# Kernel tuning notes

Measured on AMD Instinct MI355X. Metric: run time of the kernel, lower is better.

The kernel has to match this reference:

```python
import jax, jax.numpy as jnp
import numpy as np


def setup_inputs() -> dict:
    key = jax.random.key(0)
    k1, k2 = jax.random.split(key)
    x = jax.random.normal(k1, (32, 128, 112, 112), dtype=jnp.float32)
    weight = jax.random.normal(k2, (256, 128, 3, 3), dtype=jnp.float32)
    return {"x": x, "weight": weight}


def reference(x, weight):
    # Equivalent to torch unfold + einsum: valid (no padding), stride-1
    # cross-correlation conv2d with no bias.
    # x: [B, Cin, H, W], weight: [Cout, Cin, kh, kw] -> [B, Cout, H-kh+1, W-kw+1]
    return jax.lax.conv_general_dilated(
        x, weight,
        window_strides=(1, 1),
        padding="VALID",
        dimension_numbers=("NCHW", "OIHW", "NCHW"),
    )
```

## Files before the change

kernel.cpp:

```cpp
#include <hip/hip_runtime.h>

typedef __attribute__((ext_vector_type(8))) short short8;
typedef __attribute__((ext_vector_type(4))) float f32x4;
typedef unsigned int u32;

#define CIN   128
#define COUT  256
#define H     112
#define W     112
#define OH    110
#define OW    110
#define KHW   9
#define TH    8
#define TW    32
#define IWW   34
#define NPIX  340
#define XB    (NPIX*8*16)
#define WB    16384
#define ROWB  (IWW*128)

__device__ __forceinline__ short f2b(float f) {
  unsigned u = __builtin_bit_cast(unsigned, f);
  unsigned r = (u + 0x7FFFu + ((u >> 16) & 1u)) >> 16;
  return (short)r;
}

__device__ __forceinline__ void gload16(const void* g, void* l) {
  __builtin_amdgcn_global_load_lds(
      (const __attribute__((address_space(1))) u32*)g,
      (__attribute__((address_space(3))) u32*)l, 16, 0, 0);
}


template<bool XT, bool WT>
__global__ __launch_bounds__(256, 2)
void conv_main(const float* __restrict__ x, const float* __restrict__ wgt,
               const short* __restrict__ wt, const short* __restrict__ xt,
               const short* __restrict__ zp, float* __restrict__ out) {
  __shared__ __align__(16) char smem[XB + 2*WB];
  char* sx = smem;
  char* sw = smem + XB;

  const int tid = threadIdx.x;

  const int nb  = gridDim.x;
  const int swz = (blockIdx.x & 7) * (nb >> 3) + (blockIdx.x >> 3);
  const int b    = swz / 112;
  const int rem  = swz - b * 112;
  const int cblk = rem / 56;
  const int rem2 = rem - cblk * 56;
  const int t_w  = rem2 / 14;
  const int t_h  = rem2 - t_w * 14;
  const int h0 = t_h * TH, w0 = t_w * TW;

  auto stage_x = [&](int hh) {
    if (XT) {
      const short* xtb = xt + (size_t)b * (H*W*CIN);
      #pragma unroll
      for (int it = 0; it < 11; ++it) {
        int u = it*256 + tid;
        if (u < 8*NPIX) {
          int p = u >> 3;
          int iy = p / IWW, ix = p - iy * IWW;
          int Geff = (u & 7) ^ (ix & 7);
          int gy = h0 + iy, gx = w0 + ix;
          const short* src = (gy < H && gx < W)
              ? xtb + ((size_t)gy*W + gx)*CIN + hh*64 + Geff*8
              : zp;
          gload16(src, sx + u*16);
        }
      }
    } else {
      const float* xh = x + (size_t)b * CIN * (H*W) + (size_t)(hh*64) * (H*W);
      for (int u = tid; u < 8 * NPIX; u += 256) {
        int G = u / NPIX, p = u - G * NPIX;
        int iy = p / IWW, ix = p - iy * IWW;
        int gy = h0 + iy, gx = w0 + ix;
        short8 v = {0,0,0,0,0,0,0,0};
        if (gy < H && gx < W) {
          const float* s = xh + (size_t)(G*8) * (H*W) + gy * W + gx;
          #pragma unroll
          for (int j = 0; j < 8; ++j) v[j] = f2b(s[j * (H*W)]);
        }
        *(short8*)(sx + p*128 + ((G ^ (ix & 7)) << 4)) = v;
      }
    }
  };

  int wslot16[4], wgoff[4];
  #pragma unroll
  for (int it = 0; it < 4; ++it) {
    int slot = it*256 + tid;
    int c = slot >> 3, gsw = (slot & 7) ^ (c & 7);
    wslot16[it] = slot * 16;
    wgoff[it]   = (cblk*128 + c) * CIN + gsw * 8;
  }
  auto stage_w = [&](int tap, int hh, int buf) {
    if (WT) {
      const short* base = wt + tap*(COUT*CIN) + hh*64;
      #pragma unroll
      for (int it = 0; it < 4; ++it)
        gload16(base + wgoff[it], sw + buf*WB + wslot16[it]);
    } else {
      #pragma unroll
      for (int it = 0; it < 4; ++it) {
        int slot = it*256 + tid;
        int c = slot >> 3, gsw = (slot & 7) ^ (c & 7);
        int cout = cblk*128 + c;
        short8 v;
        #pragma unroll
        for (int j = 0; j < 8; ++j) {
          int cin = hh*64 + gsw*8 + j;
          v[j] = f2b(wgt[cout*(CIN*KHW) + cin*KHW + tap]);
        }
        *(short8*)(sw + buf*WB + slot*16) = v;
      }
    }
  };

  const int lane = tid & 63;
  const int wid  = tid >> 6;
  const int wm = wid >> 1;
  const int wn = wid & 1;
  const int l15 = lane & 15;
  const int kgrp = lane >> 4;
  const int l7 = l15 & 7;

  const char* abase[2];
  const char* bbase[2][3];
  #pragma unroll
  for (int s = 0; s < 2; ++s) {
    const int g = s*4 + kgrp;
    abase[s] = sw + (wm*64 + l15)*128 + ((g ^ l7) << 4);
    #pragma unroll
    for (int kw = 0; kw < 3; ++kw) {
      const int lk = l15 + kw;
      bbase[s][kw] = sx + (4*wn)*ROWB + lk*128 + ((g ^ (lk & 7)) << 4);
    }
  }

  f32x4 acc[4][8] = {};

  stage_x(0);
  stage_w(0, 0, 0);
  __syncthreads();

  #pragma unroll
  for (int st = 0; st < 18; ++st) {
    const int tap = st % 9;
    const int kh = tap / 3, kw = tap - (tap/3)*3;
    const int buf = st & 1;

    if (st + 1 < 18) stage_w((st+1) % 9, (st+1) / 9, (st+1) & 1);

    #pragma unroll
    for (int s = 0; s < 2; ++s) {
      short8 a[4];
      #pragma unroll
      for (int mi = 0; mi < 4; ++mi)
        a[mi] = *(const short8*)(abase[s] + buf*WB + mi*2048);
      short8 bf[8];
      #pragma unroll
      for (int ni = 0; ni < 8; ++ni)
        bf[ni] = *(const short8*)(bbase[s][kw] + (kh + (ni >> 1))*ROWB
                                                + (ni & 1)*2048);
      __builtin_amdgcn_s_setprio(1);
      #pragma unroll
      for (int mi = 0; mi < 4; ++mi)
        #pragma unroll
        for (int ni = 0; ni < 8; ++ni)
          acc[mi][ni] = __builtin_amdgcn_mfma_f32_16x16x32_bf16(
              a[mi], bf[ni], acc[mi][ni], 0, 0, 0);
      __builtin_amdgcn_s_setprio(0);
    }

    if (st == 8) {
      __syncthreads();
      stage_x(1);
      __syncthreads();
    } else {
      __syncthreads();
    }
  }

  float* ob = out + (size_t)b * COUT * (OH*OW);
  #pragma unroll
  for (int ni = 0; ni < 8; ++ni) {
    int oh = h0 + 4*wn + (ni >> 1);
    int ow = w0 + (ni & 1)*16 + l15;
    if (oh < OH && ow < OW) {
      #pragma unroll
      for (int mi = 0; mi < 4; ++mi) {
        #pragma unroll
        for (int r = 0; r < 4; ++r) {
          int cout = cblk*128 + wm*64 + mi*16 + kgrp*4 + r;
          ob[(size_t)cout*(OH*OW) + oh*OW + ow] = acc[mi][ni][r];
        }
      }
    }
  }
}

__global__ void wprep(const float* __restrict__ wgt, short* __restrict__ wt,
                      short* __restrict__ zp) {
  int idx = blockIdx.x * 256 + threadIdx.x;
  if (idx < 128) zp[idx] = 0;
  if (idx >= KHW*COUT*CIN) return;
  int khw  = idx / (COUT*CIN);
  int rem  = idx - khw*(COUT*CIN);
  int cout = rem >> 7, cin = rem & 127;
  wt[idx] = f2b(wgt[cout*(CIN*KHW) + cin*KHW + khw]);
}

__global__ __launch_bounds__(256)
void xprep(const float* __restrict__ x, short* __restrict__ xt) {
  __shared__ short lsh[CIN * 113];
  const int bh = blockIdx.x;
  const int b = bh / H, h = bh - b * H;
  const float* src = x + ((size_t)b * CIN * H + h) * W;
  for (int u = threadIdx.x; u < CIN * W; u += 256) {
    int c = u / W, w = u - c * W;
    lsh[c * 113 + w] = f2b(src[(size_t)c * (H*W) + w]);
  }
  __syncthreads();
  short* dst = xt + (size_t)bh * (W * CIN);
  for (int o = threadIdx.x; o < W * CIN / 8; o += 256) {
    int w = o >> 4, s = o & 15;
    short8 v;
    #pragma unroll
    for (int j = 0; j < 8; ++j) v[j] = lsh[(s*8 + j) * 113 + w];
    *(short8*)(dst + o * 8) = v;
  }
}

extern "C" void kernel_launch(void* const* d_in, const int* in_sizes, int n_in,
                              void* d_out, int out_size, void* d_ws, size_t ws_size,
                              hipStream_t stream) {
  const float* x   = (const float*)d_in[0];
  const float* wgt = (const float*)d_in[1];
  float* out = (float*)d_out;
  const size_t wt_bytes = (size_t)(KHW*COUT*CIN) * sizeof(short);
  const size_t zp_bytes = 256;
  const size_t xt_bytes = (size_t)32 * H * W * CIN * sizeof(short);
  dim3 grid(3584);
  if (ws_size >= wt_bytes + zp_bytes + xt_bytes) {
    short* wt = (short*)d_ws;
    short* zp = (short*)((char*)d_ws + wt_bytes);
    short* xt = (short*)((char*)d_ws + wt_bytes + zp_bytes);
    wprep<<<(KHW*COUT*CIN + 255)/256, 256, 0, stream>>>(wgt, wt, zp);
    xprep<<<32 * H, 256, 0, stream>>>(x, xt);
    conv_main<true, true><<<grid, 256, 0, stream>>>(x, wgt, wt, xt, zp, out);
  } else if (ws_size >= wt_bytes + zp_bytes) {
    short* wt = (short*)d_ws;
    short* zp = (short*)((char*)d_ws + wt_bytes);
    wprep<<<(KHW*COUT*CIN + 255)/256, 256, 0, stream>>>(wgt, wt, zp);
    conv_main<false, true><<<grid, 256, 0, stream>>>(x, wgt, wt, nullptr, zp, out);
  } else {
    conv_main<false, false><<<grid, 256, 0, stream>>>(x, wgt, nullptr, nullptr, nullptr, out);
  }
}
```

Measured before the change: 370.6 us.

## Compute all 256 output channels per block and prefetch second input half

Each block now covers the full 256 output channels instead of 128, so the grid halves and each input tile is staged once rather than twice. Each wave's accumulator tile doubles to 8x8 MFMA fragments. The second 64-channel half of the input tile is double-buffered and loaded in chunks during the first half's taps, which removes the mid-loop stall of barrier, reload, barrier. The cost is occupancy: launch bounds drop to one block per CU, and the larger LDS and register footprint give fewer waves to hide latency. The priority hints around the MFMA bursts are also removed.

Result: slower. 441.8 us (+19.2%).

```diff
diff --git a/kernel.cpp b/kernel.cpp
--- a/kernel.cpp
+++ b/kernel.cpp
@@ -16,7 +16,7 @@
 #define IWW   34
 #define NPIX  340
 #define XB    (NPIX*8*16)
-#define WB    16384
+#define WBUF  32768
 #define ROWB  (IWW*128)
 
 __device__ __forceinline__ short f2b(float f) {
@@ -33,24 +33,22 @@
 
 
 template<bool XT, bool WT>
-__global__ __launch_bounds__(256, 2)
+__global__ __launch_bounds__(256, 1)
 void conv_main(const float* __restrict__ x, const float* __restrict__ wgt,
                const short* __restrict__ wt, const short* __restrict__ xt,
                const short* __restrict__ zp, float* __restrict__ out) {
-  __shared__ __align__(16) char smem[XB + 2*WB];
+  __shared__ __align__(16) char smem[2*XB + 2*WBUF];
   char* sx = smem;
-  char* sw = smem + XB;
+  char* sw = smem + 2*XB;
 
   const int tid = threadIdx.x;
 
   const int nb  = gridDim.x;
   const int swz = (blockIdx.x & 7) * (nb >> 3) + (blockIdx.x >> 3);
-  const int b    = swz / 112;
-  const int rem  = swz - b * 112;
-  const int cblk = rem / 56;
-  const int rem2 = rem - cblk * 56;
-  const int t_w  = rem2 / 14;
-  const int t_h  = rem2 - t_w * 14;
+  const int b    = swz / 56;
+  const int rem  = swz - b * 56;
+  const int t_w  = rem / 14;
+  const int t_h  = rem - t_w * 14;
   const int h0 = t_h * TH, w0 = t_w * TW;
 
   auto stage_x = [&](int hh) {
@@ -67,7 +65,7 @@
           const short* src = (gy < H && gx < W)
               ? xtb + ((size_t)gy*W + gx)*CIN + hh*64 + Geff*8
               : zp;
-          gload16(src, sx + u*16);
+          gload16(src, sx + hh*XB + u*16);
         }
       }
     } else {
@@ -82,46 +80,64 @@
           #pragma unroll
           for (int j = 0; j < 8; ++j) v[j] = f2b(s[j * (H*W)]);
         }
-        *(short8*)(sx + p*128 + ((G ^ (ix & 7)) << 4)) = v;
+        *(short8*)(sx + hh*XB + p*128 + ((G ^ (ix & 7)) << 4)) = v;
       }
     }
   };
 
-  int wslot16[4], wgoff[4];
+  auto stage_x1_chunk = [&](int c) {
+    if (!XT) return;
+    const short* xtb = xt + (size_t)b * (H*W*CIN);
+    const int lim = (c == 5) ? 2720 : (c + 1) * 454;
+    #pragma unroll
+    for (int q = 0; q < 2; ++q) {
+      int u = c*454 + q*256 + tid;
+      if (u < lim) {
+        int p = u >> 3;
+        int iy = p / IWW, ix = p - iy * IWW;
+        int Geff = (u & 7) ^ (ix & 7);
+        int gy = h0 + iy, gx = w0 + ix;
+        const short* src = (gy < H && gx < W)
+            ? xtb + ((size_t)gy*W + gx)*CIN + 64 + Geff*8
+            : zp;
+        gload16(src, sx + XB + u*16);
+      }
+    }
+  };
+
+  int wgoff[8];
   #pragma unroll
-  for (int it = 0; it < 4; ++it) {
+  for (int it = 0; it < 8; ++it) {
     int slot = it*256 + tid;
     int c = slot >> 3, gsw = (slot & 7) ^ (c & 7);
-    wslot16[it] = slot * 16;
-    wgoff[it]   = (cblk*128 + c) * CIN + gsw * 8;
+    wgoff[it] = c * CIN + gsw * 8;
   }
   auto stage_w = [&](int tap, int hh, int buf) {
     if (WT) {
       const short* base = wt + tap*(COUT*CIN) + hh*64;
       #pragma unroll
-      for (int it = 0; it < 4; ++it)
-        gload16(base + wgoff[it], sw + buf*WB + wslot16[it]);
+      for (int it = 0; it < 8; ++it)
+        gload16(base + wgoff[it], sw + buf*WBUF + (it*256 + tid)*16);
     } else {
       #pragma unroll
-      for (int it = 0; it < 4; ++it) {
+      for (int it = 0; it < 8; ++it) {
         int slot = it*256 + tid;
         int c = slot >> 3, gsw = (slot & 7) ^ (c & 7);
-        int cout = cblk*128 + c;
         short8 v;
         #pragma unroll
         for (int j = 0; j < 8; ++j) {
           int cin = hh*64 + gsw*8 + j;
-          v[j] = f2b(wgt[cout*(CIN*KHW) + cin*KHW + tap]);
-        }
-        *(short8*)(sw + buf*WB + slot*16) = v;
+          v[j] = f2b(wgt[c*(CIN*KHW) + cin*KHW + tap]);
+        }
+        *(short8*)(sw + buf*WBUF + slot*16) = v;
       }
     }
   };
 
   const int lane = tid & 63;
   const int wid  = tid >> 6;
-  const int wm = wid >> 1;
-  const int wn = wid & 1;
+  const int wm = wid & 1;
+  const int wn = wid >> 1;
   const int l15 = lane & 15;
   const int kgrp = lane >> 4;
   const int l7 = l15 & 7;
@@ -131,7 +147,7 @@
   #pragma unroll
   for (int s = 0; s < 2; ++s) {
     const int g = s*4 + kgrp;
-    abase[s] = sw + (wm*64 + l15)*128 + ((g ^ l7) << 4);
+    abase[s] = sw + (wm*128 + l15)*128 + ((g ^ l7) << 4);
     #pragma unroll
     for (int kw = 0; kw < 3; ++kw) {
       const int lk = l15 + kw;
@@ -139,47 +155,54 @@
     }
   }
 
-  f32x4 acc[4][8] = {};
+  f32x4 acc[8][8] = {};
 
   stage_x(0);
   stage_w(0, 0, 0);
   __syncthreads();
 
-  #pragma unroll
-  for (int st = 0; st < 18; ++st) {
-    const int tap = st % 9;
-    const int kh = tap / 3, kw = tap - (tap/3)*3;
-    const int buf = st & 1;
-
-    if (st + 1 < 18) stage_w((st+1) % 9, (st+1) / 9, (st+1) & 1);
-
-    #pragma unroll
-    for (int s = 0; s < 2; ++s) {
-      short8 a[4];
-      #pragma unroll
-      for (int mi = 0; mi < 4; ++mi)
-        a[mi] = *(const short8*)(abase[s] + buf*WB + mi*2048);
-      short8 bf[8];
-      #pragma unroll
-      for (int ni = 0; ni < 8; ++ni)
-        bf[ni] = *(const short8*)(bbase[s][kw] + (kh + (ni >> 1))*ROWB
-                                                + (ni & 1)*2048);
-      __builtin_amdgcn_s_setprio(1);
-      #pragma unroll
-      for (int mi = 0; mi < 4; ++mi)
+  #pragma unroll 1
+  for (int hh = 0; hh < 2; ++hh) {
+    const char* bbh0 = bbase[0][0] + hh*XB;
+    const int dxb = (int)(bbh0 - bbase[0][0]);
+    #pragma unroll
+    for (int tap9 = 0; tap9 < 9; ++tap9) {
+      const int kh = tap9 / 3, kw = tap9 - (tap9/3)*3;
+      const int wboff = ((hh + tap9) & 1) * WBUF;
+
+      if (!(hh == 1 && tap9 == 8)) {
+        const int ntap = (tap9 == 8) ? 0 : tap9 + 1;
+        const int nhh  = (tap9 == 8) ? hh + 1 : hh;
+        stage_w(ntap, nhh, ((hh + tap9) & 1) ^ 1);
+      }
+      if (hh == 0 && tap9 >= 2 && tap9 <= 7) stage_x1_chunk(tap9 - 2);
+
+      #pragma unroll
+      for (int s = 0; s < 2; ++s) {
+        short8 a[8];
+        #pragma unroll
+        for (int mi = 0; mi < 8; ++mi)
+          a[mi] = *(const short8*)(abase[s] + wboff + mi*2048);
+        short8 bf[8];
         #pragma unroll
         for (int ni = 0; ni < 8; ++ni)
-          acc[mi][ni] = __builtin_amdgcn_mfma_f32_16x16x32_bf16(
-              a[mi], bf[ni], acc[mi][ni], 0, 0, 0);
-      __builtin_amdgcn_s_setprio(0);
-    }
-
-    if (st == 8) {
-      __syncthreads();
-      stage_x(1);
-      __syncthreads();
-    } else {
-      __syncthreads();
+          bf[ni] = *(const short8*)(bbase[s][kw] + dxb
+                       + (kh + (ni >> 1))*ROWB + (ni & 1)*2048);
+        #pragma unroll
+        for (int mi = 0; mi < 8; ++mi)
+          #pragma unroll
+          for (int ni = 0; ni < 8; ++ni)
+            acc[mi][ni] = __builtin_amdgcn_mfma_f32_16x16x32_bf16(
+                a[mi], bf[ni], acc[mi][ni], 0, 0, 0);
+      }
+
+      if (hh == 0 && tap9 == 8 && !XT) {
+        __syncthreads();
+        stage_x(1);
+        __syncthreads();
+      } else {
+        __syncthreads();
+      }
     }
   }
 
@@ -190,10 +213,10 @@
     int ow = w0 + (ni & 1)*16 + l15;
     if (oh < OH && ow < OW) {
       #pragma unroll
-      for (int mi = 0; mi < 4; ++mi) {
+      for (int mi = 0; mi < 8; ++mi) {
         #pragma unroll
         for (int r = 0; r < 4; ++r) {
-          int cout = cblk*128 + wm*64 + mi*16 + kgrp*4 + r;
+          int cout = wm*128 + mi*16 + kgrp*4 + r;
           ob[(size_t)cout*(OH*OW) + oh*OW + ow] = acc[mi][ni][r];
         }
       }
@@ -242,7 +265,7 @@
   const size_t wt_bytes = (size_t)(KHW*COUT*CIN) * sizeof(short);
   const size_t zp_bytes = 256;
   const size_t xt_bytes = (size_t)32 * H * W * CIN * sizeof(short);
-  dim3 grid(3584);
+  dim3 grid(1792);
   if (ws_size >= wt_bytes + zp_bytes + xt_bytes) {
     short* wt = (short*)d_ws;
     short* zp = (short*)((char*)d_ws + wt_bytes);
```
